# Kernel tuning notes

Measured on AMD Instinct MI355X. Metric: run time of the kernel, lower is better.

## Reference

```python
import jax, jax.numpy as jnp
import numpy as np

P = 4       # patch size
NQ = 6      # qubits (2**6 = 64 amplitudes)
NH = 8      # classic attention heads
HD = 8      # head dim (64 / 8)
EPS = 1e-9

_SIGNS = (1.0 - 2.0 * (((np.arange(64)[:, None] >> np.arange(NQ - 1, -1, -1)[None, :]) & 1))).astype(np.float32)  # [64, 6] Z-expectation signs, wire 0 = MSB


def _ln(x, g, b, eps=1e-5):
    m = x.mean(-1, keepdims=True)
    v = x.var(-1, keepdims=True)
    return (x - m) / jnp.sqrt(v + eps) * g + b


def _rot_rx(t):
    c = jnp.cos(t / 2).astype(jnp.complex64)
    s = jnp.sin(t / 2).astype(jnp.complex64)
    return jnp.stack([jnp.stack([c, -1j * s]), jnp.stack([-1j * s, c])])


def _rot_ry(t):
    c = jnp.cos(t / 2).astype(jnp.complex64)
    s = jnp.sin(t / 2).astype(jnp.complex64)
    return jnp.stack([jnp.stack([c, -s]), jnp.stack([s, c])])


def _apply_1q(psi, g, wire):
    # psi: [bsz, 2,2,2,2,2,2]; apply 2x2 unitary g on one wire
    ax = wire + 1
    psi = jnp.moveaxis(psi, ax, -1)
    psi = jnp.einsum('ab,...b->...a', g, psi)
    return jnp.moveaxis(psi, -1, ax)


def _cnot(psi, i):
    # CNOT on adjacent wires [i, i+1]
    cax = i + 1
    p0 = jnp.take(psi, 0, axis=cax)
    p1 = jnp.take(psi, 1, axis=cax)
    p1 = jnp.flip(p1, axis=cax)  # target axis i+2 shifts to cax after removing control axis
    return jnp.stack([p0, p1], axis=cax)


def _pqc(psi, w):
    # RX+RY -> CNOT chain -> RY per layer; w: [depth, NQ, 3]
    for l in range(w.shape[0]):
        for q in range(NQ):
            psi = _apply_1q(psi, _rot_rx(w[l, q, 0]), q)
            psi = _apply_1q(psi, _rot_ry(w[l, q, 1]), q)
        for q in range(NQ - 1):
            psi = _cnot(psi, q)
        for q in range(NQ):
            psi = _apply_1q(psi, _rot_ry(w[l, q, 2]), q)
    return psi


def _probs(psi):
    f = psi.reshape(psi.shape[0], 64)
    return f.real ** 2 + f.imag ** 2


def _measure_z(psi):
    return _probs(psi) @ jnp.asarray(_SIGNS)  # [bsz, 6]


def setup_inputs() -> dict:
    key = jax.random.key(0)
    k = lambda i: jax.random.fold_in(key, i)
    n = lambda i, shp, s=0.02: jax.random.normal(k(i), shp, jnp.float32) * s
    return dict(
        x=jax.random.normal(k(0), (16, 4, 128, 128), jnp.float32),
        conv_w=n(1, (384, 4, P, P)), conv_b=jnp.zeros((384,), jnp.float32),
        ln1_g=jnp.ones(64), ln1_b=jnp.zeros(64),
        wq=n(2, (64, 64)), wk=n(3, (64, 64)), wv=n(4, (64, 64)), wo=n(5, (64, 64)), bo=jnp.zeros(64),
        ln2_g=jnp.ones(64), ln2_b=jnp.zeros(64),
        enc_w=n(6, (2, NQ, 3), 0.1), q_w=n(7, (2, NQ, 3), 0.1), k_w=n(8, (2, NQ, 3), 0.1), v_w=n(9, (2, NQ, 3), 0.1),
        meas_q_w=n(10, (NQ, 3), 0.1), meas_k_w=n(11, (NQ, 3), 0.1), meas_v_w=n(12, (NQ, 3), 0.1),
        qproj_w=n(13, (4, NQ), 0.1), qproj_b=jnp.zeros(4),
        kproj_w=n(14, (4, NQ), 0.1), kproj_b=jnp.zeros(4),
        qkln_g=jnp.ones(4), qkln_b=jnp.zeros(4),
        raw_tau=jnp.asarray(np.log(np.exp(0.5) - 1.0), jnp.float32),
        inp_scale=jnp.ones(64),
        ln3_g=jnp.ones(64), ln3_b=jnp.zeros(64),
        mlp_w1=n(15, (256, 64)), mlp_b1=jnp.zeros(256), mlp_w2=n(16, (64, 256)), mlp_b2=jnp.zeros(64),
    )


def reference(x, conv_w, conv_b, ln1_g, ln1_b, wq, wk, wv, wo, bo, ln2_g, ln2_b,
              enc_w, q_w, k_w, v_w, meas_q_w, meas_k_w, meas_v_w,
              qproj_w, qproj_b, kproj_w, kproj_b, qkln_g, qkln_b, raw_tau, inp_scale,
              ln3_g, ln3_b, mlp_w1, mlp_b1, mlp_w2, mlp_b2):
    B, C, H, W = x.shape
    Hp, Wp = H // P, W // P
    L = Hp * Wp

    # --- PatchEmbed2D: DiT-style conv tokens [B, L, 384] ---
    t384 = jax.lax.conv_general_dilated(x, conv_w, (P, P), 'VALID',
                                        dimension_numbers=('NCHW', 'OIHW', 'NCHW'))
    t384 = t384.reshape(B, -1, L).transpose(0, 2, 1) + conv_b

    # --- PatchEmbed2D: unfold -> amplitude-normalized 64-d tokens ---
    t64 = x.reshape(B, C, Hp, P, Wp, P).transpose(0, 2, 4, 1, 3, 5).reshape(B, L, C * P * P)
    t64 = t64 / (jnp.linalg.norm(t64, axis=-1, keepdims=True) + EPS)

    # --- ClassicAttention64 (manual einsum + softmax MHSA) ---
    hin = _ln(t64, ln1_g, ln1_b)
    q = (hin @ wq.T).reshape(B, L, NH, HD).transpose(0, 2, 1, 3)
    kk = (hin @ wk.T).reshape(B, L, NH, HD).transpose(0, 2, 1, 3)
    v = (hin @ wv.T).reshape(B, L, NH, HD).transpose(0, 2, 1, 3)
    logits = jnp.einsum('bhid,bhjd->bhij', q, kk) * (HD ** -0.5)
    attn = jax.nn.softmax(logits, axis=-1)
    out = jnp.einsum('bhij,bhjd->bhid', attn, v).transpose(0, 2, 1, 3).reshape(B, L, 64)
    h = t64 + (out @ wo.T + bo)

    # --- QuantumAttention64 (QSANN, RBF kernel attention) ---
    xq = _ln(h, ln2_g, ln2_b) * inp_scale
    st = xq.reshape(B * L, 64)
    st = st / (jnp.linalg.norm(st, axis=-1, keepdims=True) + EPS)
    psi0 = st.astype(jnp.complex64).reshape((B * L,) + (2,) * NQ)
    psi_enc = _pqc(psi0, enc_w)
    zq = _measure_z(_pqc(_pqc(psi_enc, q_w), meas_q_w[None]))
    zk = _measure_z(_pqc(_pqc(psi_enc, k_w), meas_k_w[None]))
    pv = _probs(_pqc(_pqc(psi_enc, v_w), meas_v_w[None]))
    v64 = (pv / (pv.sum(-1, keepdims=True) + EPS)).reshape(B, L, 64)
    qv = _ln(zq @ qproj_w.T + qproj_b, qkln_g, qkln_b).reshape(B, L, -1)
    kv = _ln(zk @ kproj_w.T + kproj_b, qkln_g, qkln_b).reshape(B, L, -1)
    tau = jax.nn.softplus(raw_tau)
    d2 = jnp.maximum((qv ** 2).sum(-1)[:, :, None] + (kv ** 2).sum(-1)[:, None, :]
                     - 2.0 * jnp.einsum('bid,bjd->bij', qv, kv), 0.0)
    alpha = jnp.exp(-d2 / tau)
    wts = alpha / (alpha.sum(-1, keepdims=True) + EPS)
    h = h + jnp.einsum('bij,bjd->bid', wts, v64)

    # --- MLP (64 -> 256 -> 64, GELU) ---
    hm = _ln(h, ln3_g, ln3_b)
    h = h + (jax.nn.gelu(hm @ mlp_w1.T + mlp_b1, approximate=True) @ mlp_w2.T + mlp_b2)

    # combine both streams into a single output tensor [B, L, 448]
    return jnp.concatenate([t384, h], axis=-1)
```

## Files before the change

### kernel.cpp

```cpp
#include <hip/hip_runtime.h>

typedef float4 f4;
#define DEV static __device__ __forceinline__

constexpr int Ln = 1024;
constexpr float EPSn = 1e-9f;

typedef __attribute__((ext_vector_type(8))) short short8;
typedef __attribute__((ext_vector_type(16))) float f32x16;
typedef __attribute__((ext_vector_type(4))) unsigned int u32x4;

constexpr size_t OFF_T64 = 0;
constexpr size_t OFF_H   = 1048576;
constexpr size_t OFF_Q   = 2097152;
constexpr size_t OFF_K   = 3145728;
constexpr size_t OFF_V   = 4194304;
constexpr size_t OFF_AO  = 5242880;
constexpr size_t OFF_TR  = 6291456;
constexpr size_t OFF_WQT = OFF_TR + 24576;
constexpr size_t OFF_WKT = OFF_WQT + 4096;
constexpr size_t OFF_WVT = OFF_WKT + 4096;
constexpr size_t OFF_WOT = OFF_WVT + 4096;
constexpr size_t OFF_U   = OFF_WOT + 4096;
constexpr size_t OFF_W2P = OFF_U + 1024;
constexpr size_t OFF_W1P = OFF_W2P + 16384;
constexpr size_t OFF_UT  = OFF_W1P + 16384;

DEV float red16(float v) {
  v += __shfl_xor(v, 1); v += __shfl_xor(v, 2);
  v += __shfl_xor(v, 4); v += __shfl_xor(v, 8);
  return v;
}

DEV unsigned int pk_bf16(float lo, float hi) {
  unsigned int r;
  asm("v_cvt_pk_bf16_f32 %0, %1, %2" : "=v"(r) : "v"(lo), "v"(hi));
  return r;
}

DEV float fast_exp2(float x) {
#if __has_builtin(__builtin_amdgcn_exp2f)
  return __builtin_amdgcn_exp2f(x);
#else
  return __expf(x * 0.6931471805599453f);
#endif
}

DEV void cmulc(float ar, float ai, float br, float bi, float& cr, float& ci) {
  cr = ar * br - ai * bi; ci = ar * bi + ai * br;
}
DEV void mat2mul(const float* A, const float* B, float* C) {
  for (int i = 0; i < 2; ++i)
    for (int j = 0; j < 2; ++j) {
      float sr = 0.f, si = 0.f;
      for (int kk = 0; kk < 2; ++kk) {
        float pr, pi;
        cmulc(A[(i * 2 + kk) * 2], A[(i * 2 + kk) * 2 + 1],
              B[(kk * 2 + j) * 2], B[(kk * 2 + j) * 2 + 1], pr, pi);
        sr += pr; si += pi;
      }
      C[(i * 2 + j) * 2] = sr; C[(i * 2 + j) * 2 + 1] = si;
    }
}

__global__ __launch_bounds__(256) void prep_all_kernel(
    const float* __restrict__ conv_w, const float* __restrict__ wq,
    const float* __restrict__ wk, const float* __restrict__ wv,
    const float* __restrict__ wo, const float* __restrict__ w1,
    const float* __restrict__ w2,
    const float* __restrict__ enc_w, const float* __restrict__ q_w,
    const float* __restrict__ k_w, const float* __restrict__ v_w,
    const float* __restrict__ mq, const float* __restrict__ mk,
    const float* __restrict__ mv, float* __restrict__ ws) {
  __shared__ float Ulds[288];
  int bx = blockIdx.x;
  int tid = threadIdx.x;
  if (bx < 288) {
    int g = bx * 256 + tid;
    if (g < 24576) {
      int kk = g / 384, o = g % 384;
      ws[OFF_TR + g] = conv_w[o * 64 + kk];
    } else if (g < 40960) {
      int i = g - 24576;
      int m = i >> 12;
      int r = i & 4095;
      int d = r >> 6, o = r & 63;
      const float* src = m == 0 ? wq : m == 1 ? wk : m == 2 ? wv : wo;
      ws[OFF_WQT + i] = src[o * 64 + d];
    } else if (g < 57344) {
      int i = g - 40960;
      int u4 = i >> 8, r = i & 255, o = r >> 2, j = r & 3;
      ws[OFF_W2P + i] = w2[o * 256 + u4 * 4 + j];
    } else if (g < 73728) {
      int i = g - 57344;
      int d4 = i >> 10, r = i & 1023, u = r >> 2, j = r & 3;
      ws[OFF_W1P + i] = w1[u * 64 + d4 * 4 + j];
    }
    return;
  }
  int ub = bx - 288;
  int branch = ub >> 2, quad = ub & 3;
  const float* bw = branch == 0 ? q_w : branch == 1 ? k_w : v_w;
  const float* mw = branch == 0 ? mq : branch == 1 ? mk : mv;
  if (tid < 36) {
    int blk = tid / 6, wire = tid % 6;
    auto W = [&](int l, int t) -> float {
      if (l <= 1) return enc_w[(l * 6 + wire) * 3 + t];
      if (l <= 3) return bw[((l - 2) * 6 + wire) * 3 + t];
      return mw[wire * 3 + t];
    };
    auto mk_rx = [](float th, float* M) {
      float c = cosf(0.5f * th), s = sinf(0.5f * th);
      M[0] = c; M[1] = 0; M[2] = 0; M[3] = -s; M[4] = 0; M[5] = -s; M[6] = c; M[7] = 0;
    };
    auto mk_ry = [](float th, float* M) {
      float c = cosf(0.5f * th), s = sinf(0.5f * th);
      M[0] = c; M[1] = 0; M[2] = -s; M[3] = 0; M[4] = s; M[5] = 0; M[6] = c; M[7] = 0;
    };
    float R[8];
    if (blk == 0) {
      float A[8], Bx[8];
      mk_ry(W(0, 1), A); mk_rx(W(0, 0), Bx);
      mat2mul(A, Bx, R);
    } else if (blk <= 4) {
      float A[8], Bx[8], C[8], T[8];
      mk_ry(W(blk, 1), A); mk_rx(W(blk, 0), Bx); mk_ry(W(blk - 1, 2), C);
      mat2mul(Bx, C, T); mat2mul(A, T, R);
    } else {
      mk_ry(W(4, 2), R);
    }
#pragma unroll
    for (int t = 0; t < 8; ++t) Ulds[(blk * 6 + wire) * 8 + t] = R[t];
  }
  __syncthreads();
  if (tid >= 64) return;
  int s = tid & 3;
  int lane = tid;
  int c = quad * 16 + (tid >> 2);
  bool bit1 = (s & 2) != 0;
  bool bit0 = (s & 1) != 0;
  float re[16], im[16];
#pragma unroll
  for (int i = 0; i < 16; ++i) { re[i] = (s * 16 + i == c) ? 1.f : 0.f; im[i] = 0.f; }
#pragma unroll 1
  for (int blk = 0; blk < 6; ++blk) {
    const float* Uw = Ulds + blk * 48;
    {
      const float* M = Uw;
      float cAr = bit1 ? M[6] : M[0], cAi = bit1 ? M[7] : M[1];
      float cBr = bit1 ? M[4] : M[2], cBi = bit1 ? M[5] : M[3];
#pragma unroll
      for (int i = 0; i < 16; ++i) {
        float pr = __shfl_xor(re[i], 2);
        float pi = __shfl_xor(im[i], 2);
        float nr = cAr * re[i] - cAi * im[i] + cBr * pr - cBi * pi;
        float ni = cAr * im[i] + cAi * re[i] + cBr * pi + cBi * pr;
        re[i] = nr; im[i] = ni;
      }
    }
    {
      const float* M = Uw + 8;
      float cAr = bit0 ? M[6] : M[0], cAi = bit0 ? M[7] : M[1];
      float cBr = bit0 ? M[4] : M[2], cBi = bit0 ? M[5] : M[3];
#pragma unroll
      for (int i = 0; i < 16; ++i) {
        float pr = __shfl_xor(re[i], 1);
        float pi = __shfl_xor(im[i], 1);
        float nr = cAr * re[i] - cAi * im[i] + cBr * pr - cBi * pi;
        float ni = cAr * im[i] + cAi * re[i] + cBr * pi + cBi * pr;
        re[i] = nr; im[i] = ni;
      }
    }
#pragma unroll
    for (int w = 2; w < 6; ++w) {
      const float* M = Uw + w * 8;
      const float m0 = M[0], m1 = M[1], m2 = M[2], m3 = M[3];
      const float m4 = M[4], m5 = M[5], m6 = M[6], m7 = M[7];
      const int mm = 8 >> (w - 2);
#pragma unroll
      for (int i = 0; i < 16; ++i) {
        if (i & mm) continue;
        int i1 = i | mm;
        float ar = re[i], ai = im[i], br = re[i1], bi = im[i1];
        re[i]  = m0 * ar - m1 * ai + m2 * br - m3 * bi;
        im[i]  = m0 * ai + m1 * ar + m2 * bi + m3 * br;
        re[i1] = m4 * ar - m5 * ai + m6 * br - m7 * bi;
        im[i1] = m4 * ai + m5 * ar + m6 * bi + m7 * br;
      }
    }
    if (blk < 5) {
      int sl = (lane & ~3) | (bit1 ? (s ^ 1) : s);
      float tr[16], ti[16];
#pragma unroll
      for (int i = 0; i < 16; ++i) {
        tr[i] = __shfl(re[i], sl);
        ti[i] = __shfl(im[i], sl);
      }
#pragma unroll
      for (int i = 0; i < 16; ++i) {
        int j = i;
        if (j & 2) j ^= 1;
        if (j & 4) j ^= 2;
        if (j & 8) j ^= 4;
        re[i] = bit0 ? tr[j ^ 8] : tr[j];
        im[i] = bit0 ? ti[j ^ 8] : ti[j];
      }
    }
  }
  float* dre = ws + OFF_UT + (size_t)branch * 8192 + c * 64 + s * 16;
  float* dim = dre + 4096;
#pragma unroll
  for (int i = 0; i < 16; i += 4) {
    f4 r4 = {re[i], re[i + 1], re[i + 2], re[i + 3]};
    f4 i4 = {im[i], im[i + 1], im[i + 2], im[i + 3]};
    *(f4*)(dre + i) = r4;
    *(f4*)(dim + i) = i4;
  }
}

__global__ __launch_bounds__(256) void patch_kernel(const float* __restrict__ x,
    const float* __restrict__ cwT, const float* __restrict__ conv_b,
    float* __restrict__ out, float* __restrict__ t64) {
  __shared__ float A[64][72];
  __shared__ float scl[64];
  int tid = threadIdx.x;
  int tb = blockIdx.x >> 1;
  int half = blockIdx.x & 1;
  int b = tb >> 4;
  int l0 = (tb & 15) << 6;
  int seg = tid & 15;
  int c = seg >> 2, ph = seg & 3;
#pragma unroll
  for (int r = 0; r < 4; ++r) {
    int tok = (tid >> 4) + (r << 4);
    int l = l0 + tok, hp = l >> 5, wp = l & 31;
    f4 v4 = *(const f4*)(x + (size_t)((b * 4 + c) * 128 + hp * 4 + ph) * 128 + wp * 4);
    A[seg * 4 + 0][tok] = v4.x;
    A[seg * 4 + 1][tok] = v4.y;
    A[seg * 4 + 2][tok] = v4.z;
    A[seg * 4 + 3][tok] = v4.w;
  }
  __syncthreads();
  if (tid < 64) {
    float ss = 0.f;
#pragma unroll
    for (int kk = 0; kk < 64; ++kk) { float vv = A[kk][tid]; ss += vv * vv; }
    scl[tid] = 1.0f / (sqrtf(ss) + EPSn);
  }
  __syncthreads();
  int t0 = tb << 6;
  if (half == 0) {
#pragma unroll
    for (int i = 0; i < 16; ++i) {
      int idx = tid + (i << 8);
      int tok = idx >> 6, kk = idx & 63;
      t64[(size_t)(t0 + tok) * 64 + kk] = A[kk][tok] * scl[tok];
    }
  }
  int tg = tid >> 4;
  int on = (tid & 15) + half * 16;
  float acc[4][12];
#pragma unroll
  for (int i = 0; i < 4; ++i)
#pragma unroll
    for (int jj = 0; jj < 12; ++jj) acc[i][jj] = 0.f;
  for (int kk = 0; kk < 64; ++kk) {
    float a[4];
#pragma unroll
    for (int i = 0; i < 4; ++i) a[i] = A[kk][tg * 4 + i];
    f4 w0 = *(const f4*)(cwT + kk * 384 + on * 12);
    f4 w1 = *(const f4*)(cwT + kk * 384 + on * 12 + 4);
    f4 w2 = *(const f4*)(cwT + kk * 384 + on * 12 + 8);
    float wv_[12] = {w0.x, w0.y, w0.z, w0.w, w1.x, w1.y, w1.z, w1.w, w2.x, w2.y, w2.z, w2.w};
#pragma unroll
    for (int i = 0; i < 4; ++i)
#pragma unroll
      for (int jj = 0; jj < 12; ++jj) acc[i][jj] += a[i] * wv_[jj];
  }
#pragma unroll
  for (int i = 0; i < 4; ++i) {
    int tok = tg * 4 + i;
    size_t basep = (size_t)(t0 + tok) * 448 + on * 12;
#pragma unroll
    for (int jj = 0; jj < 12; ++jj)
      out[basep + jj] = acc[i][jj] + conv_b[on * 12 + jj];
  }
}

__global__ __launch_bounds__(256) void qkv_kernel(const float* __restrict__ t64,
    const float* __restrict__ wqT, const float* __restrict__ wkT, const float* __restrict__ wvT,
    const float* __restrict__ g1, const float* __restrict__ b1,
    float* __restrict__ qo, float* __restrict__ ko, float* __restrict__ vo) {
  __shared__ float wS[12288];
  __shared__ float hin[16][64];
  int tid = threadIdx.x;
#pragma unroll
  for (int p = 0; p < 16; ++p) {
    int idx = p * 256 + tid;
    wS[idx] = wqT[idx];
    wS[4096 + idx] = wkT[idx];
    wS[8192 + idx] = wvT[idx];
  }
  int t0 = blockIdx.x << 4;
  int tt = tid >> 4, part = tid & 15;
  int t = t0 + tt;
  f4 xv = *(const f4*)(t64 + (size_t)t * 64 + part * 4);
  float mean = red16(xv.x + xv.y + xv.z + xv.w) * 0.015625f;
  float d0 = xv.x - mean, d1 = xv.y - mean, d2 = xv.z - mean, d3 = xv.w - mean;
  float var = red16(d0 * d0 + d1 * d1 + d2 * d2 + d3 * d3) * 0.015625f;
  float rs = rsqrtf(var + 1e-5f);
  f4 g4 = *(const f4*)(g1 + part * 4);
  f4 b4 = *(const f4*)(b1 + part * 4);
  f4 hh;
  hh.x = d0 * rs * g4.x + b4.x; hh.y = d1 * rs * g4.y + b4.y;
  hh.z = d2 * rs * g4.z + b4.z; hh.w = d3 * rs * g4.w + b4.w;
  *(f4*)&hin[tt][part * 4] = hh;
  __syncthreads();
  float qa0 = 0, qa1 = 0, qa2 = 0, qa3 = 0;
  float ka0 = 0, ka1 = 0, ka2 = 0, ka3 = 0;
  float va0 = 0, va1 = 0, va2 = 0, va3 = 0;
  for (int d = 0; d < 64; ++d) {
    float hd = hin[tt][d];
    f4 wq4 = *(const f4*)&wS[d * 64 + part * 4];
    f4 wk4 = *(const f4*)&wS[4096 + d * 64 + part * 4];
    f4 wv4 = *(const f4*)&wS[8192 + d * 64 + part * 4];
    qa0 += hd * wq4.x; qa1 += hd * wq4.y; qa2 += hd * wq4.z; qa3 += hd * wq4.w;
    ka0 += hd * wk4.x; ka1 += hd * wk4.y; ka2 += hd * wk4.z; ka3 += hd * wk4.w;
    va0 += hd * wv4.x; va1 += hd * wv4.y; va2 += hd * wv4.z; va3 += hd * wv4.w;
  }
  f4 qr = {qa0, qa1, qa2, qa3}, kr = {ka0, ka1, ka2, ka3}, vr = {va0, va1, va2, va3};
  *(f4*)(qo + (size_t)t * 64 + part * 4) = qr;
  *(f4*)(ko + (size_t)t * 64 + part * 4) = kr;
  *(f4*)(vo + (size_t)t * 64 + part * 4) = vr;
}

__global__ __launch_bounds__(256) void attn_kernel(const float* __restrict__ qg,
    const float* __restrict__ kg, const float* __restrict__ vg, float* __restrict__ ao) {
  __shared__ __align__(16) unsigned short Klds[Ln][8];
  __shared__ __align__(16) unsigned short Vt[10][1032];
  __shared__ __align__(16) unsigned short Qlds[128][8];
  int bh = blockIdx.x;
  int b = bh >> 3, hh = bh & 7;
  int tid = threadIdx.x;
  int qbase = (blockIdx.y << 7);
  const float* kb = kg + (size_t)(b * Ln) * 64 + hh * 8;
  const float* vb = vg + (size_t)(b * Ln) * 64 + hh * 8;
  const float* qb = qg + (size_t)(b * Ln + qbase) * 64 + hh * 8;
  const float SC = 0.51006944f;
#pragma unroll
  for (int p = 0; p < 8; ++p) {
    int e4 = p * 256 + tid;
    int j = e4 >> 1, part = e4 & 1;
    f4 kv = *(const f4*)(kb + (size_t)j * 64 + part * 4);
    *(uint2*)&Klds[j][part * 4] =
        make_uint2(pk_bf16(kv.x * SC, kv.y * SC), pk_bf16(kv.z * SC, kv.w * SC));
    f4 vv = *(const f4*)(vb + (size_t)j * 64 + part * 4);
    unsigned int u01 = pk_bf16(vv.x, vv.y), u23 = pk_bf16(vv.z, vv.w);
    int d0 = part * 4;
    Vt[d0 + 0][j] = (unsigned short)u01;
    Vt[d0 + 1][j] = (unsigned short)(u01 >> 16);
    Vt[d0 + 2][j] = (unsigned short)u23;
    Vt[d0 + 3][j] = (unsigned short)(u23 >> 16);
  }
#pragma unroll
  for (int p = 0; p < 4; ++p) {
    int j = p * 256 + tid;
    Vt[8][j] = 0x3F80;
    Vt[9][j] = 0;
  }
  {
    int j = tid >> 1, part = tid & 1;
    f4 qv = *(const f4*)(qb + (size_t)j * 64 + part * 4);
    *(uint2*)&Qlds[j][part * 4] = make_uint2(pk_bf16(qv.x, qv.y), pk_bf16(qv.z, qv.w));
  }
  __syncthreads();

  int l = tid & 63, w = tid >> 6;
  int lq = l & 31;
  bool lo = l < 32;
  const short8 zero8 = {0, 0, 0, 0, 0, 0, 0, 0};
  short8 qf = *(const short8*)&Qlds[w * 32 + lq][0];
  qf = lo ? qf : zero8;
  int d = lq;
  int dc = d > 9 ? 9 : d;
  int vrow0 = (l >> 5) * 8;
  f32x16 acc = {};
  const f32x16 fz = {};
  for (int t = 0; t < 32; ++t) {
    short8 kf = *(const short8*)&Klds[t * 32 + lq][0];
    kf = lo ? kf : zero8;
    f32x16 s = __builtin_amdgcn_mfma_f32_32x32x16_bf16(kf, qf, fz, 0, 0, 0);
    float p[16];
#pragma unroll
    for (int r = 0; r < 16; ++r) p[r] = fast_exp2(s[r]);
    unsigned int c0 = pk_bf16(p[0], p[1]),  c1 = pk_bf16(p[2], p[3]);
    unsigned int c2 = pk_bf16(p[4], p[5]),  c3 = pk_bf16(p[6], p[7]);
    unsigned int c4 = pk_bf16(p[8], p[9]),  c5 = pk_bf16(p[10], p[11]);
    unsigned int c6 = pk_bf16(p[12], p[13]), c7 = pk_bf16(p[14], p[15]);
    unsigned int x0 = c0, y0 = c2;
    asm("v_permlane32_swap_b32 %0, %1" : "+v"(x0), "+v"(y0));
    unsigned int x1 = c1, y1 = c3;
    asm("v_permlane32_swap_b32 %0, %1" : "+v"(x1), "+v"(y1));
    unsigned int x4 = c4, y4 = c6;
    asm("v_permlane32_swap_b32 %0, %1" : "+v"(x4), "+v"(y4));
    unsigned int x5 = c5, y5 = c7;
    asm("v_permlane32_swap_b32 %0, %1" : "+v"(x5), "+v"(y5));
    union { u32x4 u; short8 s8; } B0, B1;
    B0.u = (u32x4){x0, x1, y0, y1};
    B1.u = (u32x4){x4, x5, y4, y5};
    int jb = t * 32 + vrow0;
    short8 av0 = *(const short8*)&Vt[dc][jb];
    short8 av1 = *(const short8*)&Vt[dc][jb + 16];
    acc = __builtin_amdgcn_mfma_f32_32x32x16_bf16(av0, B0.s8, acc, 0, 0, 0);
    acc = __builtin_amdgcn_mfma_f32_32x32x16_bf16(av1, B1.s8, acc, 0, 0, 0);
  }
  float ssum = __shfl(acc[4], lq);
  float inv = 1.0f / ssum;
  f4 o = {acc[0] * inv, acc[1] * inv, acc[2] * inv, acc[3] * inv};
  float* dst = ao + (size_t)(b * Ln + qbase + w * 32 + lq) * 64 + hh * 8 + (lo ? 0 : 4);
  *(f4*)dst = o;
}

__global__ __launch_bounds__(256) void proj_st_kernel(float* __restrict__ t64st,
    const float* __restrict__ ao, const float* __restrict__ woT, const float* __restrict__ bo,
    const float* __restrict__ g2, const float* __restrict__ b2, const float* __restrict__ iscale,
    float* __restrict__ hB) {
  __shared__ float woS[4096];
  __shared__ float aos[16][64];
  int tid = threadIdx.x;
#pragma unroll
  for (int p = 0; p < 16; ++p) {
    int idx = p * 256 + tid;
    woS[idx] = woT[idx];
  }
  int t0 = blockIdx.x << 4;
  int tt = tid >> 4, part = tid & 15;
  int t = t0 + tt;
  *(f4*)&aos[tt][part * 4] = *(const f4*)(ao + (size_t)t * 64 + part * 4);
  __syncthreads();
  f4 acc;
  acc.x = bo[part * 4 + 0]; acc.y = bo[part * 4 + 1];
  acc.z = bo[part * 4 + 2]; acc.w = bo[part * 4 + 3];
  for (int d = 0; d < 64; ++d) {
    float ad = aos[tt][d];
    f4 w4 = *(const f4*)&woS[d * 64 + part * 4];
    acc.x += ad * w4.x; acc.y += ad * w4.y; acc.z += ad * w4.z; acc.w += ad * w4.w;
  }
  f4 tv = *(const f4*)(t64st + (size_t)t * 64 + part * 4);
  f4 hv = {tv.x + acc.x, tv.y + acc.y, tv.z + acc.z, tv.w + acc.w};
  *(f4*)(hB + (size_t)t * 64 + part * 4) = hv;
  float mean = red16(hv.x + hv.y + hv.z + hv.w) * 0.015625f;
  float d0 = hv.x - mean, d1 = hv.y - mean, d2 = hv.z - mean, d3 = hv.w - mean;
  float var = red16(d0 * d0 + d1 * d1 + d2 * d2 + d3 * d3) * 0.015625f;
  float rs = rsqrtf(var + 1e-5f);
  f4 g4 = *(const f4*)(g2 + part * 4);
  f4 b4 = *(const f4*)(b2 + part * 4);
  f4 is4 = *(const f4*)(iscale + part * 4);
  float x0 = (d0 * rs * g4.x + b4.x) * is4.x;
  float x1 = (d1 * rs * g4.y + b4.y) * is4.y;
  float x2 = (d2 * rs * g4.z + b4.z) * is4.z;
  float x3 = (d3 * rs * g4.w + b4.w) * is4.w;
  float nrm = sqrtf(red16(x0 * x0 + x1 * x1 + x2 * x2 + x3 * x3));
  float rn = 1.0f / (nrm + EPSn);
  f4 stv = {x0 * rn, x1 * rn, x2 * rn, x3 * rn};
  *(f4*)(t64st + (size_t)t * 64 + part * 4) = stv;
}

__global__ __launch_bounds__(256) void quantum_kernel(const float* __restrict__ st,
    const float* __restrict__ ut,
    const float* __restrict__ qproj_w, const float* __restrict__ qproj_b,
    const float* __restrict__ kproj_w, const float* __restrict__ kproj_b,
    const float* __restrict__ qkg, const float* __restrict__ qkb,
    float* __restrict__ qvb, float* __restrict__ kvb, float* __restrict__ v64) {
  __shared__ float smem[12288];
  int tid = threadIdx.x;
  int branch = blockIdx.y;
  int t0 = blockIdx.x << 6;
  const float* ub = ut + (size_t)branch * 8192;
#pragma unroll
  for (int p = 0; p < 16; ++p) {
    int idx = p * 256 + tid;
    smem[idx] = st[(size_t)t0 * 64 + idx];
    smem[4096 + idx] = ub[idx];
    smem[8192 + idx] = ub[4096 + idx];
  }
  __syncthreads();
  int o = tid & 63, tg = tid >> 6;
  float accre[16], accim[16];
#pragma unroll
  for (int i = 0; i < 16; ++i) { accre[i] = 0.f; accim[i] = 0.f; }
  for (int k4 = 0; k4 < 16; ++k4) {
    float ur[4], ui[4];
#pragma unroll
    for (int j = 0; j < 4; ++j) {
      ur[j] = smem[4096 + (k4 * 4 + j) * 64 + o];
      ui[j] = smem[8192 + (k4 * 4 + j) * 64 + o];
    }
#pragma unroll
    for (int tt = 0; tt < 16; ++tt) {
      f4 a = *(const f4*)&smem[(tg * 16 + tt) * 64 + k4 * 4];
      accre[tt] += a.x * ur[0] + a.y * ur[1] + a.z * ur[2] + a.w * ur[3];
      accim[tt] += a.x * ui[0] + a.y * ui[1] + a.z * ui[2] + a.w * ui[3];
    }
  }
  __syncthreads();
#pragma unroll
  for (int tt = 0; tt < 16; ++tt) {
    int t = tg * 16 + tt;
    smem[t * 65 + o] = accre[tt] * accre[tt] + accim[tt] * accim[tt];
  }
  __syncthreads();
  int s = tid & 3;
  int tokL = tid >> 2;
  int token = t0 + tokL;
  bool bit1 = (s & 2) != 0;
  bool bit0 = (s & 1) != 0;
  float p[16];
#pragma unroll
  for (int i = 0; i < 16; ++i) p[i] = smem[tokL * 65 + s * 16 + i];
  float lsum = 0.f;
#pragma unroll
  for (int i = 0; i < 16; ++i) lsum += p[i];
  if (branch == 2) {
    float tot = lsum;
    tot += __shfl_xor(tot, 1);
    tot += __shfl_xor(tot, 2);
    float rn = 1.0f / (tot + EPSn);
    float* dst = v64 + (size_t)token * 64 + s * 16;
#pragma unroll
    for (int i = 0; i < 16; i += 4) {
      f4 o4 = {p[i] * rn, p[i + 1] * rn, p[i + 2] * rn, p[i + 3] * rn};
      *(f4*)(dst + i) = o4;
    }
  } else {
    float lz[4] = {0.f, 0.f, 0.f, 0.f};
#pragma unroll
    for (int i = 0; i < 16; ++i) {
      lz[0] += (i & 8) ? -p[i] : p[i];
      lz[1] += (i & 4) ? -p[i] : p[i];
      lz[2] += (i & 2) ? -p[i] : p[i];
      lz[3] += (i & 1) ? -p[i] : p[i];
    }
    float z[6];
    float u0 = bit1 ? -lsum : lsum;
    u0 += __shfl_xor(u0, 1); u0 += __shfl_xor(u0, 2); z[0] = u0;
    float u1 = bit0 ? -lsum : lsum;
    u1 += __shfl_xor(u1, 1); u1 += __shfl_xor(u1, 2); z[1] = u1;
#pragma unroll
    for (int q = 0; q < 4; ++q) {
      float v = lz[q];
      v += __shfl_xor(v, 1); v += __shfl_xor(v, 2);
      z[2 + q] = v;
    }
    const float* pw = branch == 0 ? qproj_w : kproj_w;
    const float* pb = branch == 0 ? qproj_b : kproj_b;
    float pr4[4];
#pragma unroll
    for (int jj = 0; jj < 4; ++jj) {
      float a = pb[jj];
#pragma unroll
      for (int qq = 0; qq < 6; ++qq) a += z[qq] * pw[jj * 6 + qq];
      pr4[jj] = a;
    }
    float mean = (pr4[0] + pr4[1] + pr4[2] + pr4[3]) * 0.25f;
    float var = 0.f;
#pragma unroll
    for (int jj = 0; jj < 4; ++jj) { float dd = pr4[jj] - mean; var += dd * dd; }
    var *= 0.25f;
    float rs = rsqrtf(var + 1e-5f);
    if (s == 0) {
      f4 o4;
      o4.x = (pr4[0] - mean) * rs * qkg[0] + qkb[0];
      o4.y = (pr4[1] - mean) * rs * qkg[1] + qkb[1];
      o4.z = (pr4[2] - mean) * rs * qkg[2] + qkb[2];
      o4.w = (pr4[3] - mean) * rs * qkg[3] + qkb[3];
      *(f4*)((branch == 0 ? qvb : kvb) + (size_t)token * 4) = o4;
    }
  }
}

__global__ __launch_bounds__(256) void rbf_kernel(const float* __restrict__ qvb,
    const float* __restrict__ kvb, const float* __restrict__ v64,
    const float* __restrict__ raw_tau, float* __restrict__ pacc, float* __restrict__ pasum) {
  __shared__ __align__(16) unsigned short Vt[64][520];
  __shared__ __align__(16) unsigned short kvbs[512][8];
  __shared__ float kks[512];
  int tid = threadIdx.x;
  int q0 = blockIdx.x << 7;
  int b = q0 >> 10;
  int kc = blockIdx.y;
  float tau = log1pf(__expf(raw_tau[0]));
  const float L2E = 1.4426950408889634f;
  float sck = 2.0f * L2E / tau;
  int kbase = b * Ln + (kc << 9);
#pragma unroll
  for (int p = 0; p < 2; ++p) {
    int j = p * 256 + tid;
    f4 kv4 = *(const f4*)(kvb + (size_t)(kbase + j) * 4);
    kks[j] = (kv4.x * kv4.x + kv4.y * kv4.y + kv4.z * kv4.z + kv4.w * kv4.w) * (L2E / tau);
    *(uint4*)&kvbs[j][0] =
        make_uint4(pk_bf16(kv4.x * sck, kv4.y * sck), pk_bf16(kv4.z * sck, kv4.w * sck), 0u, 0u);
  }
#pragma unroll
  for (int it = 0; it < 32; ++it) {
    int idx = it * 256 + tid;
    int row = idx >> 4, c4 = idx & 15;
    f4 vv = *(const f4*)(v64 + (size_t)(kbase + row) * 64 + c4 * 4);
    unsigned int u01 = pk_bf16(vv.x, vv.y), u23 = pk_bf16(vv.z, vv.w);
    int d0 = c4 * 4;
    Vt[d0 + 0][row] = (unsigned short)u01;
    Vt[d0 + 1][row] = (unsigned short)(u01 >> 16);
    Vt[d0 + 2][row] = (unsigned short)u23;
    Vt[d0 + 3][row] = (unsigned short)(u23 >> 16);
  }
  __syncthreads();

  int l = tid & 63, w = tid >> 6;
  int lq = l & 31;
  bool lo = l < 32;
  bool hi = !lo;
  const short8 zero8 = {0, 0, 0, 0, 0, 0, 0, 0};
  int qtok = q0 + w * 32 + lq;
  f4 qv4 = *(const f4*)(qvb + (size_t)qtok * 4);
  union { u32x4 u; short8 s8; } Qf;
  Qf.u = (u32x4){pk_bf16(qv4.x, qv4.y), pk_bf16(qv4.z, qv4.w), 0u, 0u};
  short8 qf = lo ? Qf.s8 : zero8;
  int vrow0 = (l >> 5) * 8;
  int dbase = hi ? 4 : 0;
  f32x16 acc0 = {}, acc1 = {};
  const f32x16 fz = {};
  float dsum = 0.f;
  for (int t = 0; t < 16; ++t) {
    short8 kf = lo ? *(const short8*)&kvbs[t * 32 + lq][0] : zero8;
    f32x16 s = __builtin_amdgcn_mfma_f32_32x32x16_bf16(kf, qf, fz, 0, 0, 0);
    int rowbase = t * 32 + dbase;
    float p[16];
#pragma unroll
    for (int r = 0; r < 16; ++r) {
      float kkv = kks[rowbase + (r & 3) + 8 * (r >> 2)];
      p[r] = fast_exp2(s[r] - kkv);
      dsum += p[r];
    }
    unsigned int c0 = pk_bf16(p[0], p[1]),  c1 = pk_bf16(p[2], p[3]);
    unsigned int c2 = pk_bf16(p[4], p[5]),  c3 = pk_bf16(p[6], p[7]);
    unsigned int c4 = pk_bf16(p[8], p[9]),  c5 = pk_bf16(p[10], p[11]);
    unsigned int c6 = pk_bf16(p[12], p[13]), c7 = pk_bf16(p[14], p[15]);
    unsigned int x0 = c0, y0 = c2;
    asm("v_permlane32_swap_b32 %0, %1" : "+v"(x0), "+v"(y0));
    unsigned int x1 = c1, y1 = c3;
    asm("v_permlane32_swap_b32 %0, %1" : "+v"(x1), "+v"(y1));
    unsigned int x4 = c4, y4 = c6;
    asm("v_permlane32_swap_b32 %0, %1" : "+v"(x4), "+v"(y4));
    unsigned int x5 = c5, y5 = c7;
    asm("v_permlane32_swap_b32 %0, %1" : "+v"(x5), "+v"(y5));
    union { u32x4 u; short8 s8; } B0, B1;
    B0.u = (u32x4){x0, x1, y0, y1};
    B1.u = (u32x4){x4, x5, y4, y5};
    int jb = t * 32 + vrow0;
    short8 a00 = *(const short8*)&Vt[lq][jb];
    short8 a10 = *(const short8*)&Vt[32 + lq][jb];
    short8 a01 = *(const short8*)&Vt[lq][jb + 16];
    short8 a11 = *(const short8*)&Vt[32 + lq][jb + 16];
    acc0 = __builtin_amdgcn_mfma_f32_32x32x16_bf16(a00, B0.s8, acc0, 0, 0, 0);
    acc1 = __builtin_amdgcn_mfma_f32_32x32x16_bf16(a10, B0.s8, acc1, 0, 0, 0);
    acc0 = __builtin_amdgcn_mfma_f32_32x32x16_bf16(a01, B1.s8, acc0, 0, 0, 0);
    acc1 = __builtin_amdgcn_mfma_f32_32x32x16_bf16(a11, B1.s8, acc1, 0, 0, 0);
  }
  float dtot = dsum + __shfl_xor(dsum, 32);
  if (lo) pasum[(kc << 14) + qtok] = dtot;
  float* pa = pacc + (size_t)kc * 1048576 + (size_t)qtok * 64;
#pragma unroll
  for (int r = 0; r < 16; ++r) {
    int dd = (r & 3) + 8 * (r >> 2) + dbase;
    pa[dd] = acc0[r];
    pa[32 + dd] = acc1[r];
  }
}

__global__ __launch_bounds__(256) void m0m1_kernel(float* __restrict__ hB,
    const float* __restrict__ pacc, const float* __restrict__ pasum,
    const float* __restrict__ g3, const float* __restrict__ b3,
    const float* __restrict__ w1p, const float* __restrict__ b1v,
    float* __restrict__ hid) {
  __shared__ float hmS[16][64];
  int tid = threadIdx.x;
  int t0 = blockIdx.x << 4;
  {
    int tt = tid >> 4, part = tid & 15;
    int t = t0 + tt;
    f4 hv = *(const f4*)(hB + (size_t)t * 64 + part * 4);
    f4 p0 = *(const f4*)(pacc + (size_t)t * 64 + part * 4);
    f4 p1 = *(const f4*)(pacc + 1048576 + (size_t)t * 64 + part * 4);
    float rden = 1.0f / (pasum[t] + pasum[16384 + t] + EPSn);
    hv.x += (p0.x + p1.x) * rden; hv.y += (p0.y + p1.y) * rden;
    hv.z += (p0.z + p1.z) * rden; hv.w += (p0.w + p1.w) * rden;
    *(f4*)(hB + (size_t)t * 64 + part * 4) = hv;
    float mean = red16(hv.x + hv.y + hv.z + hv.w) * 0.015625f;
    float d0 = hv.x - mean, d1 = hv.y - mean, d2 = hv.z - mean, d3 = hv.w - mean;
    float var = red16(d0 * d0 + d1 * d1 + d2 * d2 + d3 * d3) * 0.015625f;
    float rs = rsqrtf(var + 1e-5f);
    f4 g4 = *(const f4*)(g3 + part * 4);
    f4 b4 = *(const f4*)(b3 + part * 4);
    f4 o4 = {d0 * rs * g4.x + b4.x, d1 * rs * g4.y + b4.y,
             d2 * rs * g4.z + b4.z, d3 * rs * g4.w + b4.w};
    *(f4*)&hmS[tt][part * 4] = o4;
  }
  __syncthreads();
  int u = tid;
  float wrow[64];
#pragma unroll
  for (int d4 = 0; d4 < 16; ++d4) {
    f4 w4 = *(const f4*)(w1p + d4 * 1024 + u * 4);
    wrow[d4 * 4] = w4.x; wrow[d4 * 4 + 1] = w4.y;
    wrow[d4 * 4 + 2] = w4.z; wrow[d4 * 4 + 3] = w4.w;
  }
  float bias = b1v[u];
  for (int tok = 0; tok < 16; ++tok) {
    const float* hr = hmS[tok];
    float a0 = 0.f, a1 = 0.f, a2 = 0.f, a3 = 0.f;
#pragma unroll
    for (int d = 0; d < 64; d += 4) {
      a0 += hr[d] * wrow[d];
      a1 += hr[d + 1] * wrow[d + 1];
      a2 += hr[d + 2] * wrow[d + 2];
      a3 += hr[d + 3] * wrow[d + 3];
    }
    float a = bias + ((a0 + a1) + (a2 + a3));
    float tz = 0.7978845608028654f * (a + 0.044715f * a * a * a);
    float e = __expf(2.0f * tz);
    float th = 1.0f - 2.0f / (e + 1.0f);
    hid[(size_t)(t0 + tok) * 256 + u] = 0.5f * a * (1.0f + th);
  }
}

__global__ __launch_bounds__(256) void m2_kernel(const float* __restrict__ hB,
    const float* __restrict__ hid, const float* __restrict__ w2p, const float* __restrict__ b2v,
    float* __restrict__ out) {
  __shared__ float hidS[32][256];
  int tid = threadIdx.x;
  int t0 = blockIdx.x << 5;
#pragma unroll
  for (int p = 0; p < 8; ++p) {
    int idx = p * 256 + tid;
    int tok = idx >> 6, u4 = idx & 63;
    *(f4*)&hidS[tok][u4 * 4] = *(const f4*)(hid + (size_t)(t0 + tok) * 256 + u4 * 4);
  }
  __syncthreads();
  int o = tid & 63, tg = tid >> 6;
  f4 acc[8];
#pragma unroll
  for (int tt = 0; tt < 8; ++tt) acc[tt] = {0.f, 0.f, 0.f, 0.f};
#pragma unroll 4
  for (int u4 = 0; u4 < 64; ++u4) {
    f4 wv = *(const f4*)(w2p + u4 * 256 + o * 4);
#pragma unroll
    for (int tt = 0; tt < 8; ++tt) {
      f4 hv = *(const f4*)&hidS[tg * 8 + tt][u4 * 4];
      acc[tt].x += hv.x * wv.x; acc[tt].y += hv.y * wv.y;
      acc[tt].z += hv.z * wv.z; acc[tt].w += hv.w * wv.w;
    }
  }
  float bb = b2v[o];
#pragma unroll
  for (int tt = 0; tt < 8; ++tt) {
    int t = t0 + tg * 8 + tt;
    float r = bb + ((acc[tt].x + acc[tt].y) + (acc[tt].z + acc[tt].w));
    out[(size_t)t * 448 + 384 + o] = hB[(size_t)t * 64 + o] + r;
  }
}

extern "C" void kernel_launch(void* const* d_in, const int* in_sizes, int n_in,
                              void* d_out, int out_size, void* d_ws, size_t ws_size,
                              hipStream_t stream) {
  (void)in_sizes; (void)n_in; (void)out_size; (void)ws_size;
  const float* x       = (const float*)d_in[0];
  const float* conv_w  = (const float*)d_in[1];
  const float* conv_b  = (const float*)d_in[2];
  const float* ln1_g   = (const float*)d_in[3];
  const float* ln1_b   = (const float*)d_in[4];
  const float* wq      = (const float*)d_in[5];
  const float* wk      = (const float*)d_in[6];
  const float* wv      = (const float*)d_in[7];
  const float* wo      = (const float*)d_in[8];
  const float* bo      = (const float*)d_in[9];
  const float* ln2_g   = (const float*)d_in[10];
  const float* ln2_b   = (const float*)d_in[11];
  const float* enc_w   = (const float*)d_in[12];
  const float* q_w     = (const float*)d_in[13];
  const float* k_w     = (const float*)d_in[14];
  const float* v_w     = (const float*)d_in[15];
  const float* mq_w    = (const float*)d_in[16];
  const float* mk_w    = (const float*)d_in[17];
  const float* mv_w    = (const float*)d_in[18];
  const float* qproj_w = (const float*)d_in[19];
  const float* qproj_b = (const float*)d_in[20];
  const float* kproj_w = (const float*)d_in[21];
  const float* kproj_b = (const float*)d_in[22];
  const float* qkln_g  = (const float*)d_in[23];
  const float* qkln_b  = (const float*)d_in[24];
  const float* raw_tau = (const float*)d_in[25];
  const float* iscale  = (const float*)d_in[26];
  const float* ln3_g   = (const float*)d_in[27];
  const float* ln3_b   = (const float*)d_in[28];
  const float* mlp_w1  = (const float*)d_in[29];
  const float* mlp_b1  = (const float*)d_in[30];
  const float* mlp_w2  = (const float*)d_in[31];
  const float* mlp_b2  = (const float*)d_in[32];
  float* out = (float*)d_out;
  float* ws  = (float*)d_ws;

  prep_all_kernel<<<300, 256, 0, stream>>>(conv_w, wq, wk, wv, wo, mlp_w1, mlp_w2,
                                           enc_w, q_w, k_w, v_w, mq_w, mk_w, mv_w, ws);
  patch_kernel<<<512, 256, 0, stream>>>(x, ws + OFF_TR, conv_b, out, ws + OFF_T64);
  qkv_kernel<<<1024, 256, 0, stream>>>(ws + OFF_T64, ws + OFF_WQT, ws + OFF_WKT, ws + OFF_WVT,
                                       ln1_g, ln1_b, ws + OFF_Q, ws + OFF_K, ws + OFF_V);
  attn_kernel<<<dim3(128, 8), 256, 0, stream>>>(ws + OFF_Q, ws + OFF_K, ws + OFF_V, ws + OFF_AO);
  proj_st_kernel<<<1024, 256, 0, stream>>>(ws + OFF_T64, ws + OFF_AO, ws + OFF_WOT, bo,
                                           ln2_g, ln2_b, iscale, ws + OFF_H);
  quantum_kernel<<<dim3(256, 3), 256, 0, stream>>>(ws + OFF_T64, ws + OFF_UT,
                                                   qproj_w, qproj_b, kproj_w, kproj_b,
                                                   qkln_g, qkln_b,
                                                   ws + OFF_K, ws + OFF_K + 65536, ws + OFF_Q);
  rbf_kernel<<<dim3(128, 2), 256, 0, stream>>>(ws + OFF_K, ws + OFF_K + 65536, ws + OFF_Q,
                                               raw_tau, ws + OFF_V, ws + OFF_K + 131072);
  m0m1_kernel<<<1024, 256, 0, stream>>>(ws + OFF_H, ws + OFF_V, ws + OFF_K + 131072,
                                        ln3_g, ln3_b, ws + OFF_W1P, mlp_b1, ws + OFF_Q);
  m2_kernel<<<512, 256, 0, stream>>>(ws + OFF_H, ws + OFF_Q, ws + OFF_W2P, mlp_b2, out);
}
```

Before: 186.4 us.

## Split attention over two key chunks and merge partials in projection kernel

The attention kernel now launches a third grid dimension that splits the 1024 keys into two halves of 512. Each block writes unnormalized accumulators and row sums to separate workspace buffers. The projection kernel sums both partials and divides by the combined denominator before the output projection. This doubles the block count to improve occupancy and halves per-block LDS and loop length, at the cost of extra global writes and reads for the partials. It relies on no running-max subtraction, so partial exp sums can be added directly.

```diff
diff --git a/kernel.cpp b/kernel.cpp
--- a/kernel.cpp
+++ b/kernel.cpp
@@ -25,6 +25,9 @@
 constexpr size_t OFF_W2P = OFF_U + 1024;
 constexpr size_t OFF_W1P = OFF_W2P + 16384;
 constexpr size_t OFF_UT  = OFF_W1P + 16384;
+constexpr size_t OFF_AO2 = 6500352;
+constexpr size_t OFF_DS  = 7548928;
+constexpr size_t AO_STRIDE = OFF_AO2 - OFF_AO;
 
 DEV float red16(float v) {
   v += __shfl_xor(v, 1); v += __shfl_xor(v, 2);
@@ -335,20 +338,22 @@
 }
 
 __global__ __launch_bounds__(256) void attn_kernel(const float* __restrict__ qg,
-    const float* __restrict__ kg, const float* __restrict__ vg, float* __restrict__ ao) {
-  __shared__ __align__(16) unsigned short Klds[Ln][8];
-  __shared__ __align__(16) unsigned short Vt[10][1032];
+    const float* __restrict__ kg, const float* __restrict__ vg,
+    float* __restrict__ pacc, float* __restrict__ pds) {
+  __shared__ __align__(16) unsigned short Klds[512][8];
+  __shared__ __align__(16) unsigned short Vt[10][520];
   __shared__ __align__(16) unsigned short Qlds[128][8];
   int bh = blockIdx.x;
   int b = bh >> 3, hh = bh & 7;
   int tid = threadIdx.x;
   int qbase = (blockIdx.y << 7);
-  const float* kb = kg + (size_t)(b * Ln) * 64 + hh * 8;
-  const float* vb = vg + (size_t)(b * Ln) * 64 + hh * 8;
+  int kc = blockIdx.z;
+  const float* kb = kg + (size_t)(b * Ln + (kc << 9)) * 64 + hh * 8;
+  const float* vb = vg + (size_t)(b * Ln + (kc << 9)) * 64 + hh * 8;
   const float* qb = qg + (size_t)(b * Ln + qbase) * 64 + hh * 8;
   const float SC = 0.51006944f;
 #pragma unroll
-  for (int p = 0; p < 8; ++p) {
+  for (int p = 0; p < 4; ++p) {
     int e4 = p * 256 + tid;
     int j = e4 >> 1, part = e4 & 1;
     f4 kv = *(const f4*)(kb + (size_t)j * 64 + part * 4);
@@ -363,7 +368,7 @@
     Vt[d0 + 3][j] = (unsigned short)(u23 >> 16);
   }
 #pragma unroll
-  for (int p = 0; p < 4; ++p) {
+  for (int p = 0; p < 2; ++p) {
     int j = p * 256 + tid;
     Vt[8][j] = 0x3F80;
     Vt[9][j] = 0;
@@ -386,7 +391,7 @@
   int vrow0 = (l >> 5) * 8;
   f32x16 acc = {};
   const f32x16 fz = {};
-  for (int t = 0; t < 32; ++t) {
+  for (int t = 0; t < 16; ++t) {
     short8 kf = *(const short8*)&Klds[t * 32 + lq][0];
     kf = lo ? kf : zero8;
     f32x16 s = __builtin_amdgcn_mfma_f32_32x32x16_bf16(kf, qf, fz, 0, 0, 0);
@@ -414,15 +419,17 @@
     acc = __builtin_amdgcn_mfma_f32_32x32x16_bf16(av0, B0.s8, acc, 0, 0, 0);
     acc = __builtin_amdgcn_mfma_f32_32x32x16_bf16(av1, B1.s8, acc, 0, 0, 0);
   }
-  float ssum = __shfl(acc[4], lq);
-  float inv = 1.0f / ssum;
-  f4 o = {acc[0] * inv, acc[1] * inv, acc[2] * inv, acc[3] * inv};
-  float* dst = ao + (size_t)(b * Ln + qbase + w * 32 + lq) * 64 + hh * 8 + (lo ? 0 : 4);
-  *(f4*)dst = o;
+  int token = b * Ln + qbase + w * 32 + lq;
+  f4 o = {acc[0], acc[1], acc[2], acc[3]};
+  float* pa = pacc + (size_t)kc * AO_STRIDE + (size_t)token * 64 + hh * 8 + (lo ? 0 : 4);
+  *(f4*)pa = o;
+  if (lo) pds[(size_t)(kc * 8 + hh) * 16384 + token] = acc[4];
 }
 
 __global__ __launch_bounds__(256) void proj_st_kernel(float* __restrict__ t64st,
-    const float* __restrict__ ao, const float* __restrict__ woT, const float* __restrict__ bo,
+    const float* __restrict__ pa0, const float* __restrict__ pa1,
+    const float* __restrict__ pds,
+    const float* __restrict__ woT, const float* __restrict__ bo,
     const float* __restrict__ g2, const float* __restrict__ b2, const float* __restrict__ iscale,
     float* __restrict__ hB) {
   __shared__ float woS[4096];
@@ -436,7 +443,16 @@
   int t0 = blockIdx.x << 4;
   int tt = tid >> 4, part = tid & 15;
   int t = t0 + tt;
-  *(f4*)&aos[tt][part * 4] = *(const f4*)(ao + (size_t)t * 64 + part * 4);
+  {
+    f4 a0 = *(const f4*)(pa0 + (size_t)t * 64 + part * 4);
+    f4 a1 = *(const f4*)(pa1 + (size_t)t * 64 + part * 4);
+    int hp = part >> 1;
+    float den = pds[(size_t)hp * 16384 + t] + pds[(size_t)(8 + hp) * 16384 + t];
+    float inv = 1.0f / den;
+    f4 av = {(a0.x + a1.x) * inv, (a0.y + a1.y) * inv,
+             (a0.z + a1.z) * inv, (a0.w + a1.w) * inv};
+    *(f4*)&aos[tt][part * 4] = av;
+  }
   __syncthreads();
   f4 acc;
   acc.x = bo[part * 4 + 0]; acc.y = bo[part * 4 + 1];
@@ -814,8 +830,10 @@
   patch_kernel<<<512, 256, 0, stream>>>(x, ws + OFF_TR, conv_b, out, ws + OFF_T64);
   qkv_kernel<<<1024, 256, 0, stream>>>(ws + OFF_T64, ws + OFF_WQT, ws + OFF_WKT, ws + OFF_WVT,
                                        ln1_g, ln1_b, ws + OFF_Q, ws + OFF_K, ws + OFF_V);
-  attn_kernel<<<dim3(128, 8), 256, 0, stream>>>(ws + OFF_Q, ws + OFF_K, ws + OFF_V, ws + OFF_AO);
-  proj_st_kernel<<<1024, 256, 0, stream>>>(ws + OFF_T64, ws + OFF_AO, ws + OFF_WOT, bo,
+  attn_kernel<<<dim3(128, 8, 2), 256, 0, stream>>>(ws + OFF_Q, ws + OFF_K, ws + OFF_V,
+                                                   ws + OFF_AO, ws + OFF_DS);
+  proj_st_kernel<<<1024, 256, 0, stream>>>(ws + OFF_T64, ws + OFF_AO, ws + OFF_AO2,
+                                           ws + OFF_DS, ws + OFF_WOT, bo,
                                            ln2_g, ln2_b, iscale, ws + OFF_H);
   quantum_kernel<<<dim3(256, 3), 256, 0, stream>>>(ws + OFF_T64, ws + OFF_UT,
                                                    qproj_w, qproj_b, kproj_w, kproj_b,
```

Result: no change. 186.8 us (+0.2%).
